# Performance work log

Measured on AMD Instinct MI355X. Metric: run time of the kernel, lower is better.

## Reference

```python
import jax, jax.numpy as jnp
import numpy as np

SUB1 = 0.5
SUB2 = 0.2

def setup_inputs() -> dict:
    key = jax.random.key(0)
    kx, kw, kb = jax.random.split(key, 3)
    x = jax.random.normal(kx, (32, 16, 256, 256), dtype=jnp.float32)
    # Conv2d weight [C_out, C_in, K, K], PyTorch default init scale ~ 1/sqrt(fan_in)
    fan_in = 16 * 3 * 3
    bound = 1.0 / np.sqrt(fan_in)
    conv_weight = jax.random.uniform(kw, (16, 16, 3, 3), dtype=jnp.float32, minval=-bound, maxval=bound)
    conv_bias = jax.random.uniform(kb, (16,), dtype=jnp.float32, minval=-bound, maxval=bound)
    return {"x": x, "conv_weight": conv_weight, "conv_bias": conv_bias}

def mish(v):
    # mish(v) = v * tanh(softplus(v))
    return v * jnp.tanh(jax.nn.softplus(v))

def reference(x, conv_weight, conv_bias):
    # valid conv, stride 1, NCHW / OIHW
    y = jax.lax.conv_general_dilated(
        x, conv_weight,
        window_strides=(1, 1),
        padding='VALID',
        dimension_numbers=('NCHW', 'OIHW', 'NCHW'))
    y = y + conv_bias[None, :, None, None]
    y = y - (SUB1 + SUB2)
    return mish(y)
```

## Files before the change

kernel.cpp:

```cpp
#include <hip/hip_runtime.h>
#include <hip/hip_bf16.h>

constexpr int N  = 32;
constexpr int C  = 16;
constexpr int H  = 256;
constexpr int W  = 256;
constexpr int CO = 16;
constexpr int KS = 3;
constexpr int OH = 254;
constexpr int OW = 254;

constexpr float SUBV = 0.7f;

constexpr int TW = 64;
constexpr int TH = 16;
constexpr int CICHUNK = 4;
constexpr int IN_W = TW + 4;
constexpr int IN_H = TH + 2;
constexpr int QUADS_PER_ROW = IN_W / 4;
constexpr int STAGE_QUADS = CICHUNK * IN_H * QUADS_PER_ROW;

__global__ void reorder_weights(const float* __restrict__ w,
                                const float* __restrict__ b,
                                float* __restrict__ wr) {
    const int t = threadIdx.x;
    for (int i = t; i < C * KS * KS * CO; i += blockDim.x) {
        const int co   = i % CO;
        const int rest = i / CO;
        const int kx   = rest % 3;
        const int ky   = (rest / 3) % 3;
        const int ci   = rest / 9;
        wr[i] = w[((co * C + ci) * KS + ky) * KS + kx];
    }
    if (t < CO) wr[C * KS * KS * CO + t] = b[t] - SUBV;
}

__launch_bounds__(256, 4)
__global__ void conv_mish(const float* __restrict__ x,
                          const float* __restrict__ wr,
                          float* __restrict__ out) {
    __shared__ float lds[CICHUNK * IN_H * IN_W];

    const int tid = threadIdx.x;
    const int x0  = blockIdx.x * TW;
    const int oy0 = blockIdx.y * TH;
    const int n   = blockIdx.z;

    const int col = tid & 15;
    const int py  = tid >> 4;
    const int px0 = col * 4;

    float acc[4][CO];
#pragma unroll
    for (int p = 0; p < 4; ++p)
#pragma unroll
        for (int co = 0; co < CO; ++co) acc[p][co] = 0.0f;

    for (int cc = 0; cc < C; cc += CICHUNK) {
        if (cc) __syncthreads();

        const float* src = x + ((size_t)(n * C + cc) * H) * W;
        for (int q = tid; q < STAGE_QUADS; q += 256) {
            const int ciq  = q / (IN_H * QUADS_PER_ROW);
            int rem        = q - ciq * (IN_H * QUADS_PER_ROW);
            const int row  = rem / QUADS_PER_ROW;
            const int quad = rem - row * QUADS_PER_ROW;
            int iy = oy0 + row;      if (iy > H - 1) iy = H - 1;
            int ix = x0 + quad * 4;  if (ix > W - 4) ix = W - 4;
            const float4 v = *(const float4*)(src + ((size_t)ciq * H + iy) * W + ix);
            *(float4*)(&lds[(ciq * IN_H + row) * IN_W + quad * 4]) = v;
        }
        __syncthreads();

#pragma unroll
        for (int ci = 0; ci < CICHUNK; ++ci) {
            float in[3][6];
#pragma unroll
            for (int r = 0; r < 3; ++r) {
                const float* p = &lds[(ci * IN_H + py + r) * IN_W + px0];
                const float4 a = *(const float4*)p;
                const float2 bl = *(const float2*)(p + 4);
                in[r][0] = a.x; in[r][1] = a.y; in[r][2] = a.z; in[r][3] = a.w;
                in[r][4] = bl.x; in[r][5] = bl.y;
            }
            const float* wp = wr + (cc + ci) * 9 * CO;
#pragma unroll
            for (int ky = 0; ky < 3; ++ky) {
#pragma unroll
                for (int kx = 0; kx < 3; ++kx) {
#pragma unroll
                    for (int co = 0; co < CO; ++co) {
                        const float wv = wp[(ky * 3 + kx) * CO + co];
#pragma unroll
                        for (int p = 0; p < 4; ++p)
                            acc[p][co] = fmaf(in[ky][kx + p], wv, acc[p][co]);
                    }
                }
            }
        }
    }

    const int oy = oy0 + py;
    if (oy < OH) {
#pragma unroll
        for (int co = 0; co < CO; ++co) {
            const float bias = wr[C * KS * KS * CO + co];
            float* orow = out + ((size_t)(n * CO + co) * OH + oy) * OW;
#pragma unroll
            for (int p = 0; p < 4; ++p) {
                const int ox = x0 + px0 + p;
                if (ox < OW) {
                    const float v  = acc[p][co] + bias;
                    const float vc = fminf(v, 15.0f);
                    const float e  = __expf(vc);
                    const float z  = 1.0f + e;
                    const float z2 = z * z;
                    const float t  = __fdividef(z2 - 1.0f, z2 + 1.0f);
                    orow[ox] = v * t;
                }
            }
        }
    }
}

extern "C" void kernel_launch(void* const* d_in, const int* in_sizes, int n_in,
                              void* d_out, int out_size, void* d_ws, size_t ws_size,
                              hipStream_t stream) {
    const float* x = (const float*)d_in[0];
    const float* w = (const float*)d_in[1];
    const float* b = (const float*)d_in[2];
    float* out = (float*)d_out;
    float* wr  = (float*)d_ws;

    hipLaunchKernelGGL(reorder_weights, dim3(1), dim3(256), 0, stream, w, b, wr);

    dim3 grid((OW + TW - 1) / TW, (OH + TH - 1) / TH, N);
    hipLaunchKernelGGL(conv_mish, grid, dim3(256), 0, stream, x, wr, out);
}
```

Measured before the change: 351.8 us.

## Rewrite conv as implicit GEMM on bf16 MFMA with channel-last LDS tile

Replaces the scalar FP32 FMA direct convolution with an implicit-GEMM formulation using the 16x16x32 bf16 MFMA instruction. Weights are packed as bf16 A fragments held in registers, and the input tile is converted to bf16 and stored channel-interleaved (NHWC-like, padded stride) in LDS so each B fragment is a single 16-byte load. The loop over channel chunks and its repeated syncs go away in favour of one staging pass. Rounding both activations and weights to bf16 reduces accuracy and may exceed tolerance.

```diff
diff --git a/kernel.cpp b/kernel.cpp
--- a/kernel.cpp
+++ b/kernel.cpp
@@ -1,122 +1,153 @@
 #include <hip/hip_runtime.h>
 #include <hip/hip_bf16.h>
 
-constexpr int N  = 32;
-constexpr int C  = 16;
-constexpr int H  = 256;
-constexpr int W  = 256;
-constexpr int CO = 16;
-constexpr int KS = 3;
-constexpr int OH = 254;
-constexpr int OW = 254;
-
+constexpr int N   = 32;
+constexpr int C   = 16;
+constexpr int H   = 256;
+constexpr int W   = 256;
+constexpr int CO  = 16;
+constexpr int OH  = 254;
+constexpr int OW  = 254;
 constexpr float SUBV = 0.7f;
 
-constexpr int TW = 64;
-constexpr int TH = 16;
-constexpr int CICHUNK = 4;
-constexpr int IN_W = TW + 4;
-constexpr int IN_H = TH + 2;
-constexpr int QUADS_PER_ROW = IN_W / 4;
-constexpr int STAGE_QUADS = CICHUNK * IN_H * QUADS_PER_ROW;
+constexpr int KPAD = 160;
+
+constexpr int TY    = 14;
+constexpr int TIN_Y = TY + 2;
+constexpr int TX    = 64;
+constexpr int TIN_X = TX + 2;
+constexpr int XS    = 24;
+constexpr int ROW_US = TIN_X * XS;
+
+using short8  = __attribute__((ext_vector_type(8))) short;
+using floatx4 = __attribute__((ext_vector_type(4))) float;
+
+__device__ inline uint bf16u(float f) {
+    uint u = __builtin_bit_cast(uint, f);
+    u += 0x7fffu + ((u >> 16) & 1u);
+    return u >> 16;
+}
 
 __global__ void reorder_weights(const float* __restrict__ w,
                                 const float* __restrict__ b,
-                                float* __restrict__ wr) {
+                                ushort* __restrict__ wr) {
     const int t = threadIdx.x;
-    for (int i = t; i < C * KS * KS * CO; i += blockDim.x) {
-        const int co   = i % CO;
-        const int rest = i / CO;
-        const int kx   = rest % 3;
-        const int ky   = (rest / 3) % 3;
-        const int ci   = rest / 9;
-        wr[i] = w[((co * C + ci) * KS + ky) * KS + kx];
+    for (int i = t; i < CO * KPAD; i += 256) {
+        const int co = i / KPAD;
+        const int k  = i - co * KPAD;
+        ushort v = 0;
+        if (k < 144) {
+            const int pair = k >> 4;
+            const int ci   = k & 15;
+            const int ky   = pair / 3;
+            const int kx   = pair - 3 * ky;
+            v = (ushort)bf16u(w[((co * C + ci) * 3 + ky) * 3 + kx]);
+        }
+        wr[i] = v;
     }
-    if (t < CO) wr[C * KS * KS * CO + t] = b[t] - SUBV;
+    if (t < CO) ((float*)(wr + CO * KPAD))[t] = b[t] - SUBV;
 }
 
-__launch_bounds__(256, 4)
-__global__ void conv_mish(const float* __restrict__ x,
-                          const float* __restrict__ wr,
+__launch_bounds__(256, 3)
+__global__ void conv_mfma(const float* __restrict__ x,
+                          const ushort* __restrict__ wr,
                           float* __restrict__ out) {
-    __shared__ float lds[CICHUNK * IN_H * IN_W];
+    __shared__ ushort lds[TIN_Y * ROW_US];
 
-    const int tid = threadIdx.x;
-    const int x0  = blockIdx.x * TW;
-    const int oy0 = blockIdx.y * TH;
-    const int n   = blockIdx.z;
+    const int tid  = threadIdx.x;
+    const int lane = tid & 63;
+    const int wave = tid >> 6;
+    const int quad = lane >> 4;
+    const int n    = lane & 15;
 
-    const int col = tid & 15;
-    const int py  = tid >> 4;
-    const int px0 = col * 4;
+    const int x0 = blockIdx.x * TX;
+    const int y0 = blockIdx.y * TY;
+    const int ni = blockIdx.z;
 
-    float acc[4][CO];
-#pragma unroll
-    for (int p = 0; p < 4; ++p)
-#pragma unroll
-        for (int co = 0; co < CO; ++co) acc[p][co] = 0.0f;
+    short8 afrag[5];
+    {
+        const ushort* wbase = wr + n * KPAD + quad * 8;
+        #pragma unroll
+        for (int c = 0; c < 5; ++c)
+            afrag[c] = *(const short8*)(wbase + c * 32);
+    }
+    float bias_j[4];
+    {
+        const float* bp = (const float*)(wr + CO * KPAD);
+        const float4 bv = *(const float4*)(bp + quad * 4);
+        bias_j[0] = bv.x; bias_j[1] = bv.y; bias_j[2] = bv.z; bias_j[3] = bv.w;
+    }
+    int boff[5];
+    #pragma unroll
+    for (int c = 0; c < 5; ++c) {
+        int pair = 2 * c + (quad >> 1);
+        if (pair > 8) pair = 8;
+        const int ky = pair / 3;
+        const int kx = pair - 3 * ky;
+        boff[c] = ky * ROW_US + (n + kx) * XS + (quad & 1) * 8;
+    }
+    size_t obase[4];
+    const int oxv = x0 + wave * 16 + n;
+    const bool oxok = oxv < OW;
+    #pragma unroll
+    for (int j = 0; j < 4; ++j)
+        obase[j] = ((size_t)(ni * CO + quad * 4 + j)) * OH * OW + oxv;
 
-    for (int cc = 0; cc < C; cc += CICHUNK) {
-        if (cc) __syncthreads();
-
-        const float* src = x + ((size_t)(n * C + cc) * H) * W;
-        for (int q = tid; q < STAGE_QUADS; q += 256) {
-            const int ciq  = q / (IN_H * QUADS_PER_ROW);
-            int rem        = q - ciq * (IN_H * QUADS_PER_ROW);
-            const int row  = rem / QUADS_PER_ROW;
-            const int quad = rem - row * QUADS_PER_ROW;
-            int iy = oy0 + row;      if (iy > H - 1) iy = H - 1;
-            int ix = x0 + quad * 4;  if (ix > W - 4) ix = W - 4;
-            const float4 v = *(const float4*)(src + ((size_t)ciq * H + iy) * W + ix);
-            *(float4*)(&lds[(ciq * IN_H + row) * IN_W + quad * 4]) = v;
-        }
-        __syncthreads();
-
-#pragma unroll
-        for (int ci = 0; ci < CICHUNK; ++ci) {
-            float in[3][6];
-#pragma unroll
-            for (int r = 0; r < 3; ++r) {
-                const float* p = &lds[(ci * IN_H + py + r) * IN_W + px0];
-                const float4 a = *(const float4*)p;
-                const float2 bl = *(const float2*)(p + 4);
-                in[r][0] = a.x; in[r][1] = a.y; in[r][2] = a.z; in[r][3] = a.w;
-                in[r][4] = bl.x; in[r][5] = bl.y;
+    {
+        const float* xs = x + (size_t)ni * C * H * W;
+        for (int sp = tid; sp < (TIN_Y * TIN_X) / 2; sp += 256) {
+            const int s  = sp * 2;
+            const int yy = s / TIN_X;
+            const int xx = s - yy * TIN_X;
+            const int iy  = (y0 + yy < H - 1) ? (y0 + yy) : (H - 1);
+            const int ixp = (x0 + xx < W - 2) ? (x0 + xx) : (W - 2);
+            const float* src = xs + (size_t)iy * W + ixp;
+            uint a[8], b[8];
+            #pragma unroll
+            for (int ci = 0; ci < C; ci += 2) {
+                const float2 p0 = *(const float2*)(src + (size_t)ci * H * W);
+                const float2 p1 = *(const float2*)(src + (size_t)(ci + 1) * H * W);
+                a[ci >> 1] = bf16u(p0.x) | (bf16u(p1.x) << 16);
+                b[ci >> 1] = bf16u(p0.y) | (bf16u(p1.y) << 16);
             }
-            const float* wp = wr + (cc + ci) * 9 * CO;
-#pragma unroll
-            for (int ky = 0; ky < 3; ++ky) {
-#pragma unroll
-                for (int kx = 0; kx < 3; ++kx) {
-#pragma unroll
-                    for (int co = 0; co < CO; ++co) {
-                        const float wv = wp[(ky * 3 + kx) * CO + co];
-#pragma unroll
-                        for (int p = 0; p < 4; ++p)
-                            acc[p][co] = fmaf(in[ky][kx + p], wv, acc[p][co]);
-                    }
-                }
-            }
+            ushort* d0 = &lds[(yy * TIN_X + xx) * XS];
+            ((uint4*)d0)[0] = make_uint4(a[0], a[1], a[2], a[3]);
+            ((uint4*)d0)[1] = make_uint4(a[4], a[5], a[6], a[7]);
+            ushort* d1 = d0 + XS;
+            ((uint4*)d1)[0] = make_uint4(b[0], b[1], b[2], b[3]);
+            ((uint4*)d1)[1] = make_uint4(b[4], b[5], b[6], b[7]);
         }
     }
+    __syncthreads();
 
-    const int oy = oy0 + py;
-    if (oy < OH) {
-#pragma unroll
-        for (int co = 0; co < CO; ++co) {
-            const float bias = wr[C * KS * KS * CO + co];
-            float* orow = out + ((size_t)(n * CO + co) * OH + oy) * OW;
-#pragma unroll
-            for (int p = 0; p < 4; ++p) {
-                const int ox = x0 + px0 + p;
-                if (ox < OW) {
-                    const float v  = acc[p][co] + bias;
+    const ushort* wcol = lds + wave * 16 * XS;
+    #pragma unroll 1
+    for (int r = 0; r < TY; r += 2) {
+        floatx4 acc0 = {0.f, 0.f, 0.f, 0.f};
+        floatx4 acc1 = {0.f, 0.f, 0.f, 0.f};
+        const ushort* b0 = wcol + r * ROW_US;
+        const ushort* b1 = b0 + ROW_US;
+        #pragma unroll
+        for (int c = 0; c < 5; ++c) {
+            const short8 f0 = *(const short8*)(b0 + boff[c]);
+            const short8 f1 = *(const short8*)(b1 + boff[c]);
+            acc0 = __builtin_amdgcn_mfma_f32_16x16x32_bf16(afrag[c], f0, acc0, 0, 0, 0);
+            acc1 = __builtin_amdgcn_mfma_f32_16x16x32_bf16(afrag[c], f1, acc1, 0, 0, 0);
+        }
+        #pragma unroll
+        for (int rr = 0; rr < 2; ++rr) {
+            const int oy = y0 + r + rr;
+            if (oy < OH && oxok) {
+                const floatx4 av = rr ? acc1 : acc0;
+                #pragma unroll
+                for (int j = 0; j < 4; ++j) {
+                    const float v  = av[j] + bias_j[j];
                     const float vc = fminf(v, 15.0f);
                     const float e  = __expf(vc);
                     const float z  = 1.0f + e;
                     const float z2 = z * z;
                     const float t  = __fdividef(z2 - 1.0f, z2 + 1.0f);
-                    orow[ox] = v * t;
+                    out[obase[j] + (size_t)oy * OW] = v * t;
                 }
             }
         }
@@ -130,10 +161,10 @@
     const float* w = (const float*)d_in[1];
     const float* b = (const float*)d_in[2];
     float* out = (float*)d_out;
-    float* wr  = (float*)d_ws;
+    ushort* wr = (ushort*)d_ws;
 
     hipLaunchKernelGGL(reorder_weights, dim3(1), dim3(256), 0, stream, w, b, wr);
 
-    dim3 grid((OW + TW - 1) / TW, (OH + TH - 1) / TH, N);
-    hipLaunchKernelGGL(conv_mish, grid, dim3(256), 0, stream, x, wr, out);
+    dim3 grid(OW / TX + 1, (OH + TY - 1) / TY, N);
+    hipLaunchKernelGGL(conv_mfma, grid, dim3(256), 0, stream, x, wr, out);
 }
```

New measurement: 286.8 us. 1.23x faster.
